# Optimization experiments

Measured on AMD Instinct MI355X. Metric: run time of the kernel, lower is better.

## Reference

```python
import jax, jax.numpy as jnp
import numpy as np

B, C, H, W = 256, 32, 64, 64


def _affine_grid(theta, Hs, Ws):
    # theta: [B,2,3]; align_corners=False (PyTorch default). Returns [B,H,W,2] with (x,y) order.
    xs = (2.0 * jnp.arange(Ws, dtype=theta.dtype) + 1.0) / Ws - 1.0  # [W]
    ys = (2.0 * jnp.arange(Hs, dtype=theta.dtype) + 1.0) / Hs - 1.0  # [H]
    Xg, Yg = jnp.meshgrid(xs, ys)                                    # [H,W] each
    base = jnp.stack([Xg, Yg, jnp.ones_like(Xg)], axis=-1)           # [H,W,3]
    return jnp.einsum('bij,hwj->bhwi', theta, base)                  # [B,H,W,2]


def _grid_sample_bilinear(x, grid):
    # x: [B,C,H,W]; grid: [B,H,W,2] normalized (x,y); bilinear, zero padding, align_corners=False.
    Bs, Cs, Hs, Ws = x.shape
    gx = (grid[..., 0] + 1.0) * (Ws * 0.5) - 0.5
    gy = (grid[..., 1] + 1.0) * (Hs * 0.5) - 0.5
    x0 = jnp.floor(gx); y0 = jnp.floor(gy)
    x1 = x0 + 1.0;      y1 = y0 + 1.0
    wx1 = gx - x0; wx0 = 1.0 - wx1
    wy1 = gy - y0; wy0 = 1.0 - wy1

    def corner(xf, yf, w):
        valid = (xf >= 0) & (xf <= Ws - 1) & (yf >= 0) & (yf <= Hs - 1)
        xi = jnp.clip(xf, 0, Ws - 1).astype(jnp.int32)
        yi = jnp.clip(yf, 0, Hs - 1).astype(jnp.int32)
        vals = jax.vmap(lambda img, yy, xx: img[:, yy, xx])(x, yi, xi)  # [B,C,H,W] gather
        return vals * (w * valid)[:, None, :, :]

    return (corner(x0, y0, wx0 * wy0) + corner(x1, y0, wx1 * wy0)
            + corner(x0, y1, wx0 * wy1) + corner(x1, y1, wx1 * wy1))


def reference(x, w1, b1, w2, b2, w3, b3):
    Bs = x.shape[0]
    xs = x.reshape(Bs, -1)
    xs = jax.nn.relu(xs @ w1.T + b1)
    xs = jax.nn.relu(xs @ w2.T + b2)
    theta = (xs @ w3.T + b3).reshape(Bs, 2, 3)
    grid = _affine_grid(theta, x.shape[2], x.shape[3])
    return _grid_sample_bilinear(x, grid)


def setup_inputs() -> dict:
    key = jax.random.key(0)
    ks = jax.random.split(key, 8)
    fan1 = C * H * W
    x = jax.random.normal(ks[0], (B, C, H, W), dtype=jnp.float32)
    w1 = jax.random.normal(ks[1], (32, fan1), dtype=jnp.float32) / np.sqrt(fan1)
    b1 = jax.random.normal(ks[2], (32,), dtype=jnp.float32) * 0.01
    w2 = jax.random.normal(ks[3], (32, 32), dtype=jnp.float32) / np.sqrt(32.0)
    b2 = jax.random.normal(ks[4], (32,), dtype=jnp.float32) * 0.01
    w3 = jax.random.normal(ks[5], (6, 32), dtype=jnp.float32) * 0.001
    identity = jnp.array([1.0, 0.0, 0.0, 0.0, 1.0, 0.0], dtype=jnp.float32)
    b3 = identity + jax.random.normal(ks[6], (6,), dtype=jnp.float32) * 0.01
    return {"x": x, "w1": w1, "b1": b1, "w2": w2, "b2": b2, "w3": w3, "b3": b3}
```

## Files before the change

### kernel.cpp

```cpp
#include <hip/hip_runtime.h>
#include <hip/hip_bf16.h>


#define K_TOT 131072
#define KC    256
#define PKN   1024
#define STRB  ((size_t)PKN * 32)

typedef short s16x8 __attribute__((ext_vector_type(8)));
typedef float f32x4 __attribute__((ext_vector_type(4)));

__device__ __forceinline__ short f2bf(float f) {
    return __builtin_bit_cast(short, __float2bfloat16(f));
}

__device__ __forceinline__ s16x8 cvt8(float4 a, float4 b) {
    s16x8 r;
    r[0] = f2bf(a.x); r[1] = f2bf(a.y); r[2] = f2bf(a.z); r[3] = f2bf(a.w);
    r[4] = f2bf(b.x); r[5] = f2bf(b.y); r[6] = f2bf(b.z); r[7] = f2bf(b.w);
    return r;
}

__device__ __forceinline__ void gload_lds16(const float* g, float* l) {
    __builtin_amdgcn_global_load_lds(
        (const __attribute__((address_space(1))) void*)(g),
        (__attribute__((address_space(3))) void*)(l),
        16, 0, 0);
}

__global__ __launch_bounds__(256) void st_p1k(const float* __restrict__ x,
                                              const float* __restrict__ w1,
                                              float* __restrict__ partial) {
    __shared__ __align__(16) float xbuf[3][16 * KC];

    const int bid  = blockIdx.x;
    const int t    = threadIdx.x;
    const int wv   = t >> 6;
    const int lane = t & 63;
    const int m    = lane & 15;
    const int kb   = lane >> 4;
    const int jh   = wv & 1;
    const int kh   = wv >> 1;

    const int xcd  = bid & 7;
    const int q    = bid >> 3;
    const int kc   = xcd * 64 + (q >> 1);
    const int half = q & 1;
    const size_t k0 = (size_t)kc * KC;

    const float* wq = w1 + (size_t)(jh * 16 + m) * K_TOT + k0 + (size_t)kh * 128 + kb * 8;
    float4 wr[8];
#pragma unroll
    for (int sss = 0; sss < 4; ++sss) {
        wr[2 * sss]     = *(const float4*)(wq + sss * 32);
        wr[2 * sss + 1] = *(const float4*)(wq + sss * 32 + 4);
    }

#pragma unroll
    for (int pt = 0; pt < 2; ++pt) {
#pragma unroll
        for (int i2 = 0; i2 < 4; ++i2) {
            const int r = wv * 4 + i2;
            const int b0 = half * 128 + pt * 16;
            const float* gsrc = x + (size_t)(b0 + r) * K_TOT + k0 + ((lane ^ (r & 7)) << 2);
            gload_lds16(gsrc, &xbuf[pt][r * KC]);
        }
    }

    s16x8 wf[4];
#pragma unroll
    for (int sss = 0; sss < 4; ++sss) wf[sss] = cvt8(wr[2 * sss], wr[2 * sss + 1]);

    const int pk = kc * 2 + kh;
    const int sw = m & 7;

#pragma unroll
    for (int it = 0; it < 8; ++it) {
        if (it == 0)              asm volatile("s_waitcnt vmcnt(4)"  ::: "memory");
        else if (it == 1 || it == 7) asm volatile("s_waitcnt vmcnt(8)"  ::: "memory");
        else                      asm volatile("s_waitcnt vmcnt(12)" ::: "memory");
        __builtin_amdgcn_s_barrier();
        __builtin_amdgcn_sched_barrier(0);

        if (it + 2 < 8) {
            float* nbuf = xbuf[(it + 2) % 3];
            const int b0n = half * 128 + (it + 2) * 16;
#pragma unroll
            for (int i2 = 0; i2 < 4; ++i2) {
                const int r = wv * 4 + i2;
                const float* gsrc = x + (size_t)(b0n + r) * K_TOT + k0 + ((lane ^ (r & 7)) << 2);
                gload_lds16(gsrc, nbuf + r * KC);
            }
        }

        const float* xr = &xbuf[it % 3][m * KC];
        f32x4 acc = {0.f, 0.f, 0.f, 0.f};
#pragma unroll
        for (int sss = 0; sss < 4; ++sss) {
            const int gb = kh * 32 + sss * 8 + kb * 2;
            const float4 fa = *(const float4*)(xr + ((gb ^ sw) << 2));
            const float4 fb = *(const float4*)(xr + (((gb + 1) ^ sw) << 2));
            const s16x8 af = cvt8(fa, fb);
            acc = __builtin_amdgcn_mfma_f32_16x16x32_bf16(af, wf[sss], acc, 0, 0, 0);
        }

        const int b0 = half * 128 + it * 16;
        float* p0 = partial + (size_t)(b0 + kb * 4) * STRB + (size_t)pk * 32 + jh * 16 + m;
#pragma unroll
        for (int rr = 0; rr < 4; ++rr)
            p0[(size_t)rr * STRB] = acc[rr];
    }
}

__global__ __launch_bounds__(256) void st_p2k(const float* __restrict__ partial,
                                              const float* __restrict__ b1,
                                              const float* __restrict__ w2,
                                              const float* __restrict__ b2,
                                              const float* __restrict__ w3,
                                              const float* __restrict__ b3,
                                              float* __restrict__ theta) {
    const int b = blockIdx.x;
    const int t = threadIdx.x;
    const float* pb = partial + (size_t)b * STRB;

    float4 v = {0.f, 0.f, 0.f, 0.f};
#pragma unroll
    for (int i = 0; i < 32; ++i) {
        const float4 u = *(const float4*)(pb + (size_t)(i * 256 + t) * 4);
        v.x += u.x; v.y += u.y; v.z += u.z; v.w += u.w;
    }

    __shared__ float4 red[256];
    __shared__ float s1s[32];
    __shared__ float s2s[32];
    red[t] = v;
    __syncthreads();
#pragma unroll
    for (int off = 128; off >= 8; off >>= 1) {
        if (t < off) {
            float4 a = red[t];
            const float4 c = red[t + off];
            a.x += c.x; a.y += c.y; a.z += c.z; a.w += c.w;
            red[t] = a;
        }
        __syncthreads();
    }
    if (t < 8) {
        const float4 qd = red[t];
        s1s[4 * t + 0] = fmaxf(qd.x + b1[4 * t + 0], 0.f);
        s1s[4 * t + 1] = fmaxf(qd.y + b1[4 * t + 1], 0.f);
        s1s[4 * t + 2] = fmaxf(qd.z + b1[4 * t + 2], 0.f);
        s1s[4 * t + 3] = fmaxf(qd.w + b1[4 * t + 3], 0.f);
    }
    __syncthreads();
    if (t < 32) {
        float vv = b2[t];
#pragma unroll
        for (int i = 0; i < 32; ++i) vv += w2[t * 32 + i] * s1s[i];
        s2s[t] = fmaxf(vv, 0.f);
    }
    __syncthreads();
    if (t < 8) {
        float vv = 0.f;
        if (t < 6) {
            vv = b3[t];
#pragma unroll
            for (int i = 0; i < 32; ++i) vv += w3[t * 32 + i] * s2s[i];
        }
        theta[b * 8 + t] = vv;
    }
}

__global__ __launch_bounds__(256) void st_p3k(const float* __restrict__ x,
                                              const float* __restrict__ theta,
                                              float* __restrict__ out) {
    const int bid = blockIdx.x;
    const int b   = bid >> 3;
    const int h0  = (bid & 7) * 8;
    const int t   = threadIdx.x;
    const int w   = t & 63;
    const int c0  = t >> 6;

    const float* tb = theta + b * 8;
    const float t0 = tb[0], t1 = tb[1], t2 = tb[2];
    const float t3 = tb[3], t4 = tb[4], t5 = tb[5];

    for (int r = 0; r < 8; ++r) {
        const int h = h0 + r;
        const float xs = ((float)w - 31.5f) * 0.03125f;
        const float ys = ((float)h - 31.5f) * 0.03125f;
        const float gxn = fmaf(t1, ys, fmaf(t0, xs, t2));
        const float gyn = fmaf(t4, ys, fmaf(t3, xs, t5));
        const float gx = fmaf(gxn, 32.f, 31.5f);
        const float gy = fmaf(gyn, 32.f, 31.5f);
        const float x0f = floorf(gx), y0f = floorf(gy);
        const float wx1 = gx - x0f, wx0 = 1.f - wx1;
        const float wy1 = gy - y0f, wy0 = 1.f - wy1;
        const int ix = (int)x0f, iy = (int)y0f;
        const bool vx0 = (ix >= 0) && (ix < 64);
        const bool vx1 = (ix >= -1) && (ix < 63);
        const bool vy0 = (iy >= 0) && (iy < 64);
        const bool vy1 = (iy >= -1) && (iy < 63);
        const int cx0 = min(max(ix, 0), 63);
        const int cx1 = min(max(ix + 1, 0), 63);
        const int cy0 = min(max(iy, 0), 63);
        const int cy1 = min(max(iy + 1, 0), 63);
        const float w00 = wx0 * wy0 * ((vx0 && vy0) ? 1.f : 0.f);
        const float w10 = wx1 * wy0 * ((vx1 && vy0) ? 1.f : 0.f);
        const float w01 = wx0 * wy1 * ((vx0 && vy1) ? 1.f : 0.f);
        const float w11 = wx1 * wy1 * ((vx1 && vy1) ? 1.f : 0.f);
        const int r0 = cy0 * 64, r1 = cy1 * 64;
#pragma unroll
        for (int i = 0; i < 8; ++i) {
            const int c = c0 + 4 * i;
            const float* img = x + (((size_t)b * 32 + c) << 12);
            const float v = w00 * img[r0 + cx0] + w10 * img[r0 + cx1]
                          + w01 * img[r1 + cx0] + w11 * img[r1 + cx1];
            __builtin_nontemporal_store(v, &out[(((size_t)b * 32 + c) << 12) + h * 64 + w]);
        }
    }
}

extern "C" void kernel_launch(void* const* d_in, const int* in_sizes, int n_in,
                              void* d_out, int out_size, void* d_ws, size_t ws_size,
                              hipStream_t stream) {
    const float* x  = (const float*)d_in[0];
    const float* w1 = (const float*)d_in[1];
    const float* b1 = (const float*)d_in[2];
    const float* w2 = (const float*)d_in[3];
    const float* b2 = (const float*)d_in[4];
    const float* w3 = (const float*)d_in[5];
    const float* b3 = (const float*)d_in[6];
    float* out = (float*)d_out;
    float* ws  = (float*)d_ws;
    float* partial = ws;
    float* theta   = ws + (size_t)256 * STRB;

    st_p1k<<<1024, 256, 0, stream>>>(x, w1, partial);
    st_p2k<<<256, 256, 0, stream>>>(partial, b1, w2, b2, w3, b3, theta);
    st_p3k<<<2048, 256, 0, stream>>>(x, theta, out);
}
```

Baseline: 87.88 us.

## Split first GEMV by batch groups with longer K chunks per block

Reworks the first-layer split-K decomposition. Each block now handles a 1024-wide K chunk for one group of 16 batch rows, accumulating across four sub-chunks in registers, instead of a 256-wide chunk across 128 batch rows. This cuts the partial-sum buffer by four times, shrinking both the partial writes and the reduction reads in the second kernel. The cost is that each block loads four times more w1 data into registers, w1 is re-read by 16 batch-group blocks, and twice as many blocks are launched.

```diff
diff --git a/kernel.cpp b/kernel.cpp
--- a/kernel.cpp
+++ b/kernel.cpp
@@ -3,8 +3,8 @@
 
 
 #define K_TOT 131072
-#define KC    256
-#define PKN   1024
+#define KCB   1024
+#define PKN   256
 #define STRB  ((size_t)PKN * 32)
 
 typedef short s16x8 __attribute__((ext_vector_type(8)));
@@ -31,7 +31,7 @@
 __global__ __launch_bounds__(256) void st_p1k(const float* __restrict__ x,
                                               const float* __restrict__ w1,
                                               float* __restrict__ partial) {
-    __shared__ __align__(16) float xbuf[3][16 * KC];
+    __shared__ __align__(16) float xbuf[3][16 * 256];
 
     const int bid  = blockIdx.x;
     const int t    = threadIdx.x;
@@ -42,18 +42,24 @@
     const int jh   = wv & 1;
     const int kh   = wv >> 1;
 
-    const int xcd  = bid & 7;
-    const int q    = bid >> 3;
-    const int kc   = xcd * 64 + (q >> 1);
-    const int half = q & 1;
-    const size_t k0 = (size_t)kc * KC;
-
-    const float* wq = w1 + (size_t)(jh * 16 + m) * K_TOT + k0 + (size_t)kh * 128 + kb * 8;
-    float4 wr[8];
-#pragma unroll
-    for (int sss = 0; sss < 4; ++sss) {
-        wr[2 * sss]     = *(const float4*)(wq + sss * 32);
-        wr[2 * sss + 1] = *(const float4*)(wq + sss * 32 + 4);
+    const int xcd = bid & 7;
+    const int q   = bid >> 3;
+    const int kc  = xcd * 16 + (q >> 4);
+    const int bg  = q & 15;
+    const int b0  = bg * 16;
+    const size_t k0 = (size_t)kc * KCB;
+
+    s16x8 wf[16];
+    {
+        const float* wq = w1 + (size_t)(jh * 16 + m) * K_TOT + k0 + (size_t)kh * 128 + kb * 8;
+#pragma unroll
+        for (int it = 0; it < 4; ++it) {
+#pragma unroll
+            for (int sss = 0; sss < 4; ++sss) {
+                const float* wp = wq + it * 256 + sss * 32;
+                wf[it * 4 + sss] = cvt8(*(const float4*)wp, *(const float4*)(wp + 4));
+            }
+        }
     }
 
 #pragma unroll
@@ -61,55 +67,48 @@
 #pragma unroll
         for (int i2 = 0; i2 < 4; ++i2) {
             const int r = wv * 4 + i2;
-            const int b0 = half * 128 + pt * 16;
-            const float* gsrc = x + (size_t)(b0 + r) * K_TOT + k0 + ((lane ^ (r & 7)) << 2);
-            gload_lds16(gsrc, &xbuf[pt][r * KC]);
-        }
-    }
-
-    s16x8 wf[4];
-#pragma unroll
-    for (int sss = 0; sss < 4; ++sss) wf[sss] = cvt8(wr[2 * sss], wr[2 * sss + 1]);
-
-    const int pk = kc * 2 + kh;
+            const float* gsrc = x + (size_t)(b0 + r) * K_TOT + k0 + pt * 256
+                                  + ((lane ^ (r & 7)) << 2);
+            gload_lds16(gsrc, &xbuf[pt][r * 256]);
+        }
+    }
+
     const int sw = m & 7;
-
-#pragma unroll
-    for (int it = 0; it < 8; ++it) {
-        if (it == 0)              asm volatile("s_waitcnt vmcnt(4)"  ::: "memory");
-        else if (it == 1 || it == 7) asm volatile("s_waitcnt vmcnt(8)"  ::: "memory");
-        else                      asm volatile("s_waitcnt vmcnt(12)" ::: "memory");
+    f32x4 acc = {0.f, 0.f, 0.f, 0.f};
+
+#pragma unroll
+    for (int it = 0; it < 4; ++it) {
+        if (it < 3) asm volatile("s_waitcnt vmcnt(4)" ::: "memory");
+        else        asm volatile("s_waitcnt vmcnt(0)" ::: "memory");
         __builtin_amdgcn_s_barrier();
         __builtin_amdgcn_sched_barrier(0);
 
-        if (it + 2 < 8) {
-            float* nbuf = xbuf[(it + 2) % 3];
-            const int b0n = half * 128 + (it + 2) * 16;
+        if (it + 2 < 4) {
 #pragma unroll
             for (int i2 = 0; i2 < 4; ++i2) {
                 const int r = wv * 4 + i2;
-                const float* gsrc = x + (size_t)(b0n + r) * K_TOT + k0 + ((lane ^ (r & 7)) << 2);
-                gload_lds16(gsrc, nbuf + r * KC);
+                const float* gsrc = x + (size_t)(b0 + r) * K_TOT + k0 + (it + 2) * 256
+                                      + ((lane ^ (r & 7)) << 2);
+                gload_lds16(gsrc, &xbuf[(it + 2) % 3][r * 256]);
             }
         }
 
-        const float* xr = &xbuf[it % 3][m * KC];
-        f32x4 acc = {0.f, 0.f, 0.f, 0.f};
+        const float* xr = &xbuf[it % 3][m * 256];
 #pragma unroll
         for (int sss = 0; sss < 4; ++sss) {
             const int gb = kh * 32 + sss * 8 + kb * 2;
             const float4 fa = *(const float4*)(xr + ((gb ^ sw) << 2));
             const float4 fb = *(const float4*)(xr + (((gb + 1) ^ sw) << 2));
             const s16x8 af = cvt8(fa, fb);
-            acc = __builtin_amdgcn_mfma_f32_16x16x32_bf16(af, wf[sss], acc, 0, 0, 0);
-        }
-
-        const int b0 = half * 128 + it * 16;
-        float* p0 = partial + (size_t)(b0 + kb * 4) * STRB + (size_t)pk * 32 + jh * 16 + m;
-#pragma unroll
-        for (int rr = 0; rr < 4; ++rr)
-            p0[(size_t)rr * STRB] = acc[rr];
-    }
+            acc = __builtin_amdgcn_mfma_f32_16x16x32_bf16(af, wf[it * 4 + sss], acc, 0, 0, 0);
+        }
+    }
+
+    const int pk = kc * 2 + kh;
+    float* p0 = partial + (size_t)(b0 + kb * 4) * STRB + (size_t)pk * 32 + jh * 16 + m;
+#pragma unroll
+    for (int rr = 0; rr < 4; ++rr)
+        p0[(size_t)rr * STRB] = acc[rr];
 }
 
 __global__ __launch_bounds__(256) void st_p2k(const float* __restrict__ partial,
@@ -125,7 +124,7 @@
 
     float4 v = {0.f, 0.f, 0.f, 0.f};
 #pragma unroll
-    for (int i = 0; i < 32; ++i) {
+    for (int i = 0; i < 8; ++i) {
         const float4 u = *(const float4*)(pb + (size_t)(i * 256 + t) * 4);
         v.x += u.x; v.y += u.y; v.z += u.z; v.w += u.w;
     }
@@ -236,7 +235,7 @@
     float* partial = ws;
     float* theta   = ws + (size_t)256 * STRB;
 
-    st_p1k<<<1024, 256, 0, stream>>>(x, w1, partial);
+    st_p1k<<<2048, 256, 0, stream>>>(x, w1, partial);
     st_p2k<<<256, 256, 0, stream>>>(partial, b1, w2, b2, w3, b3, theta);
     st_p3k<<<2048, 256, 0, stream>>>(x, theta, out);
 }
```

After: 92.44 us. 1.05x slower.
